# Kernel tuning notes

Hardware: AMD Instinct MI355X
Metric: run time of the kernel (lower is better)

Reference implementation:

```python
import math
import jax, jax.numpy as jnp
import numpy as np

B, T, S, D, H, L, DFF, IN, PERIOD = 16, 600, 600, 1024, 8, 8, 4096, 52, 25
HD = D // H
NEG = -1e9


def _param(key, name, shape, scale=0.02):
    k = jax.random.fold_in(key, hash(name) % (2**31))
    return jax.random.normal(k, shape, dtype=jnp.float32) * scale


def setup_inputs() -> dict:
    key = jax.random.key(0)
    k1, k2, k3 = jax.random.split(key, 3)
    inp = {}
    inp["x"] = jax.random.normal(k1, (B, T, IN), dtype=jnp.float32)
    inp["memory"] = jax.random.normal(k2, (B, S, D), dtype=jnp.float32)
    inp["timesteps"] = jax.random.randint(k3, (B,), 0, 1000, dtype=jnp.int32)

    # Periodic positional encoding buffer: sinusoidal over one period, tiled.
    pos = jnp.arange(PERIOD, dtype=jnp.float32)[:, None]
    div = jnp.exp(jnp.arange(0, D, 2, dtype=jnp.float32) * (-math.log(10000.0) / D))
    pe_p = jnp.zeros((PERIOD, D), dtype=jnp.float32)
    pe_p = pe_p.at[:, 0::2].set(jnp.sin(pos * div)).at[:, 1::2].set(jnp.cos(pos * div))
    inp["pe"] = jnp.tile(pe_p, (T // PERIOD + 1, 1))[:T]  # [T, D]

    # ALiBi-style periodic bias (vectorized form of init_bi_biased_mask_faceformer).
    # alibi[h,i,j] = -slope_h * floor((i-j)/period) for j<=i, -slope_h*floor((j-i-1)/period) for j>i
    slopes = jnp.array([0.5 ** (h + 1) for h in range(H)], dtype=jnp.float32)
    di = jnp.arange(T)[:, None] - jnp.arange(T)[None, :]
    steps = jnp.where(di >= 0, di // PERIOD, (-di - 1) // PERIOD).astype(jnp.float32)
    inp["alibi"] = -slopes[:, None, None] * steps[None]  # [H, T, T]

    # Parameters
    inp["W_in"] = _param(key, "W_in", (D, IN))
    inp["b_in"] = jnp.zeros((D,), jnp.float32)
    inp["te_W1"] = _param(key, "te_W1", (D, D))
    inp["te_b1"] = jnp.zeros((D,), jnp.float32)
    inp["te_W2"] = _param(key, "te_W2", (D, D))
    inp["te_b2"] = jnp.zeros((D,), jnp.float32)
    for nm, shape in [
        ("sa_Wqkv", (L, 3 * D, D)), ("sa_bqkv", (L, 3 * D)),
        ("sa_Wo", (L, D, D)), ("sa_bo", (L, D)),
        ("ca_Wqkv", (L, 3 * D, D)), ("ca_bqkv", (L, 3 * D)),
        ("ca_Wo", (L, D, D)), ("ca_bo", (L, D)),
        ("ff_W1", (L, DFF, D)), ("ff_b1", (L, DFF)),
        ("ff_W2", (L, D, DFF)), ("ff_b2", (L, D)),
    ]:
        inp[nm] = _param(key, nm, shape)
    for nm in ["ln1_g", "ln2_g", "ln3_g"]:
        inp[nm] = jnp.ones((L, D), jnp.float32)
    for nm in ["ln1_b", "ln2_b", "ln3_b"]:
        inp[nm] = jnp.zeros((L, D), jnp.float32)
    inp["W_out"] = _param(key, "W_out", (IN, D))
    inp["b_out"] = jnp.zeros((IN,), jnp.float32)
    return inp


def _ln(x, g, b, eps=1e-5):
    mu = jnp.mean(x, axis=-1, keepdims=True)
    var = jnp.mean(jnp.square(x - mu), axis=-1, keepdims=True)
    return (x - mu) * jax.lax.rsqrt(var + eps) * g + b


def _mha(q_in, kv_in, Wqkv, bqkv, Wo, bo, bias):
    # q_in: [B,Tq,D]; kv_in: [B,Tk,D]; bias broadcastable to [B,H,Tq,Tk]
    Wq, Wk, Wv = jnp.split(Wqkv, 3, axis=0)
    bq, bk, bv = jnp.split(bqkv, 3, axis=0)
    Bn, Tq, _ = q_in.shape
    Tk = kv_in.shape[1]
    q = (q_in @ Wq.T + bq).reshape(Bn, Tq, H, HD).transpose(0, 2, 1, 3)
    k = (kv_in @ Wk.T + bk).reshape(Bn, Tk, H, HD).transpose(0, 2, 1, 3)
    v = (kv_in @ Wv.T + bv).reshape(Bn, Tk, H, HD).transpose(0, 2, 1, 3)
    scores = jnp.einsum("bhqd,bhkd->bhqk", q, k) / math.sqrt(HD) + bias
    attn = jax.nn.softmax(scores, axis=-1)
    out = jnp.einsum("bhqk,bhkd->bhqd", attn, v)
    out = out.transpose(0, 2, 1, 3).reshape(Bn, Tq, D)
    return out @ Wo.T + bo


def reference(x, memory, timesteps, pe, alibi, W_in, b_in, te_W1, te_b1, te_W2, te_b2,
              sa_Wqkv, sa_bqkv, sa_Wo, sa_bo, ca_Wqkv, ca_bqkv, ca_Wo, ca_bo,
              ff_W1, ff_b1, ff_W2, ff_b2, ln1_g, ln1_b, ln2_g, ln2_b, ln3_g, ln3_b,
              W_out, b_out):
    # --- timestep embedding (DDPM sinusoidal + 2-layer SiLU MLP) ---
    half = D // 2
    exponent = jnp.exp(-math.log(10000.0) * jnp.arange(half, dtype=jnp.float32) / (half - 1.0))
    emb = timesteps.astype(jnp.float32)[:, None] * exponent[None, :]
    t_emb = jnp.concatenate([jnp.sin(emb), jnp.cos(emb)], axis=-1)  # [B, D]
    t_emb = jax.nn.silu(t_emb @ te_W1.T + te_b1) @ te_W2.T + te_b2
    adapter = t_emb[:, None, :]  # [B, 1, D] adapter token

    # --- input projection + periodic positional encoding ---
    h = x @ W_in.T + b_in + pe[None]  # [B, T, D]

    # --- attention biases (adapter column is always attendable => zero bias) ---
    sa_bias = jnp.concatenate([jnp.zeros((H, T, 1), jnp.float32), alibi], axis=-1)[None]  # [1,H,T,1+T]
    eye = jnp.eye(T, S, dtype=jnp.float32)
    mem_bias = jnp.where(eye > 0, 0.0, NEG)  # FaceFormer diagonal-only memory mask
    mem_bias = jnp.concatenate([jnp.zeros((T, 1), jnp.float32), mem_bias], axis=-1)[None, None]  # [1,1,T,1+S]

    # --- stacked decoder layers (post-norm, adapter prepended to K/V) ---
    for l in range(L):
        x_adpt = jnp.concatenate([adapter, h], axis=1)  # [B, 1+T, D]
        h = _ln(h + _mha(h, x_adpt, sa_Wqkv[l], sa_bqkv[l], sa_Wo[l], sa_bo[l], sa_bias), ln1_g[l], ln1_b[l])
        mem_adpt = jnp.concatenate([adapter, memory], axis=1)  # [B, 1+S, D]
        h = _ln(h + _mha(h, mem_adpt, ca_Wqkv[l], ca_bqkv[l], ca_Wo[l], ca_bo[l], mem_bias), ln2_g[l], ln2_b[l])
        ff = jax.nn.relu(h @ ff_W1[l].T + ff_b1[l]) @ ff_W2[l].T + ff_b2[l]
        h = _ln(h + ff, ln3_g[l], ln3_b[l])

    return h @ W_out.T + b_out  # [B, T, IN]
```

## Files before the change

### kernel.cpp

```cpp
#include <hip/hip_runtime.h>
#include <stdint.h>

#define B_ 16
#define T_ 600
#define S_ 600
#define D_ 1024
#define H_ 8
#define HD_ 128
#define L_ 8
#define DFF_ 4096
#define IN_ 52
#define TP1 601
#define MTOK 9600
#define MPAD 9728
#define VTK 608

typedef unsigned short u16;
typedef float f32x4 __attribute__((ext_vector_type(4)));
typedef __bf16 bf16x8 __attribute__((ext_vector_type(8)));

__device__ __forceinline__ u16 f2bf(float f){
  union { float f; unsigned u; } v; v.f = f;
  v.u += 0x7FFFu + ((v.u >> 16) & 1u);
  return (u16)(v.u >> 16);
}
__device__ __forceinline__ float bf2f(u16 h){
  union { unsigned u; float f; } v; v.u = ((unsigned)h) << 16;
  return v.f;
}
__device__ __forceinline__ void gld_lds16(const void* g, void* l){
  __builtin_amdgcn_global_load_lds(
      (const __attribute__((address_space(1))) void*)(uintptr_t)g,
      (__attribute__((address_space(3))) void*)(uintptr_t)l, 16, 0, 0);
}
__device__ __forceinline__ f32x4 MM(bf16x8 a, bf16x8 b, f32x4 c){
  return __builtin_amdgcn_mfma_f32_16x16x32_bf16(a, b, c, 0, 0, 0);
}
#define BAR() asm volatile("s_barrier" ::: "memory")

template<int EPI>
__global__ __launch_bounds__(512, 2)
void k_gemm256(const u16* __restrict__ A, const u16* __restrict__ W,
               const float* __restrict__ bias, void* __restrict__ Cout,
               int N, int K){
  __shared__ u16 lds[65536];
  const int t = threadIdx.x;
  const int w = t >> 6, l = t & 63;
  const int lr = l & 15, lg = l >> 4;
  const int wr = w >> 2, wc = w & 3;

  int lin = blockIdx.y * gridDim.x + blockIdx.x;
  const int nwg = gridDim.x * gridDim.y;
  lin = (lin & 7) * (nwg >> 3) + (lin >> 3);
  const long m0 = (long)(lin / gridDim.x) * 256;
  const long n0 = (long)(lin % gridDim.x) * 256;

  const int srow = w*8 + (l >> 3);
  const int schk = (l & 7) ^ (l >> 3);
  const u16* gA = A + (m0 + srow) * (long)K + schk * 8;
  const u16* gB = W + (n0 + srow) * (long)K + schk * 8;

  const int chk0 = ((    lg) ^ (lr & 7)) * 8;
  const int chk1 = ((4 + lg) ^ (lr & 7)) * 8;
  const int arow = (wr*128 + lr) * 64;
  const int brow = (wc*64  + lr) * 64 + 16384;

  f32x4 acc[8][4] = {};
  const int NT = K >> 6;

#define STG_A(i) gld_lds16(gA + (long)(i)*64*K + nc, (void*)(lds + nb + (i)*4096 + w*512))
#define STG_B(i) gld_lds16(gB + (long)(i)*64*K + nc, (void*)(lds + nb + 16384 + (i)*4096 + w*512))
#define LOADF(mq, CH) \
    a0 = *(const bf16x8*)(lds + bufo + arow + ((mq)*4+0)*1024 + (CH)); \
    a1 = *(const bf16x8*)(lds + bufo + arow + ((mq)*4+1)*1024 + (CH)); \
    a2 = *(const bf16x8*)(lds + bufo + arow + ((mq)*4+2)*1024 + (CH)); \
    a3 = *(const bf16x8*)(lds + bufo + arow + ((mq)*4+3)*1024 + (CH)); \
    b0 = *(const bf16x8*)(lds + bufo + brow + 0*1024 + (CH)); \
    b1 = *(const bf16x8*)(lds + bufo + brow + 1*1024 + (CH)); \
    b2 = *(const bf16x8*)(lds + bufo + brow + 2*1024 + (CH));  \
    b3 = *(const bf16x8*)(lds + bufo + brow + 3*1024 + (CH));
#define MFMA16(mq) \
    __builtin_amdgcn_s_setprio(1); \
    { const bf16x8 aa[4] = {a0,a1,a2,a3}; const bf16x8 bb4[4] = {b0,b1,b2,b3}; \
      _Pragma("unroll") for (int i_ = 0; i_ < 4; i_++) \
        _Pragma("unroll") for (int j_ = 0; j_ < 4; j_++) \
          acc[(mq)*4+i_][j_] = MM(aa[i_], bb4[j_], acc[(mq)*4+i_][j_]); } \
    __builtin_amdgcn_s_setprio(0);

  { const int nb = 0; const long nc = 0;
    STG_B(0); STG_B(1); STG_B(2); STG_B(3);
    STG_A(0); STG_A(1); STG_A(2); STG_A(3);
  }
  asm volatile("s_waitcnt vmcnt(0)" ::: "memory");
  BAR();

  int bufo = 0;
  for (int tt = 0; tt < NT; ++tt){
    const int nb = bufo ^ 32768;
    const bool st = (tt + 1 < NT);
    const long nc = (long)(tt + 1) * 64;
    bf16x8 a0,a1,a2,a3,b0,b1,b2,b3;
    LOADF(0, chk0);
    if (st){ STG_B(0); STG_B(1); STG_B(2); STG_B(3); }
    BAR();
    MFMA16(0);
    BAR();
    LOADF(0, chk1);
    if (st){ STG_A(0); STG_A(1); STG_A(2); STG_A(3); }
    BAR();
    MFMA16(0);
    BAR();
    LOADF(1, chk0);
    BAR();
    MFMA16(1);
    BAR();
    LOADF(1, chk1);
    asm volatile("s_waitcnt vmcnt(0)" ::: "memory");
    BAR();
    MFMA16(1);
    BAR();
    bufo = nb;
  }
#undef STG_A
#undef STG_B
#undef LOADF
#undef MFMA16

  const int r4 = lg * 4;
#pragma unroll
  for (int nf = 0; nf < 4; nf++){
    const int colt = wc*64 + nf*16 + lr;
    const float bv = bias[n0 + colt];
#pragma unroll
    for (int mf = 0; mf < 8; mf++){
      const int rowt = wr*128 + mf*16 + r4;
#pragma unroll
      for (int r = 0; r < 4; r++){
        float v = acc[mf][nf][r] + bv;
        if (EPI == 1) v = fmaxf(v, 0.f);
        const int row = rowt + r;
        lds[row*256 + (((colt >> 3) ^ (row & 7)) << 3) + (colt & 7)] = f2bf(v);
      }
    }
  }
  BAR();
  u16* cbase = (u16*)Cout + n0;
#pragma unroll
  for (int pass = 0; pass < 2; pass++){
#pragma unroll
    for (int it = 0; it < 8; it++){
      const int row = it*32 + w*4 + (l >> 4);
      const int ck  = (l & 15) + pass*16;
      const uint4 v = *(const uint4*)(lds + row*256 + ((ck ^ (row & 7)) << 3));
      *(uint4*)(cbase + (m0 + row) * (long)N + ck*8) = v;
    }
  }
}

template<int EPI>
__global__ __launch_bounds__(256, 4)
void k_gemm_n128(const u16* __restrict__ A, const u16* __restrict__ W,
                 const float* __restrict__ bias, void* __restrict__ Cout,
                 int N, int K){
  __shared__ u16 lds[16384];
  const int t = threadIdx.x;
  const int w = t >> 6, l = t & 63;
  const int lr = l & 15, lg = l >> 4;
  const int wr = w >> 1, wc = w & 1;

  int lin = blockIdx.y * gridDim.x + blockIdx.x;
  const int nwg = gridDim.x * gridDim.y;
  lin = (lin & 7) * (nwg >> 3) + (lin >> 3);
  const long m0 = (long)(lin / gridDim.x) * 128;
  const long n0 = (long)(lin % gridDim.x) * 128;

  const int schk = (t & 3) ^ ((t >> 3) & 3);
  const u16* gA = A + (m0 + (t >> 2)) * (long)K + schk * 8;
  const u16* gB = W + (n0 + (t >> 2)) * (long)K + schk * 8;

  const int ch = (lg ^ ((lr >> 1) & 3)) * 8;
  const int aoff = wr*2048 + lr*32 + ch;
  const int boff = 4096 + wc*2048 + lr*32 + ch;

  f32x4 acc[4][4] = {};
  const int NT = K >> 5;

#define STG128(nb, nc) \
    gld_lds16(gA + (nc),              (void*)(lds + (nb) + 0    + w*512)); \
    gld_lds16(gA + 64*(long)K + (nc), (void*)(lds + (nb) + 2048 + w*512)); \
    gld_lds16(gB + (nc),              (void*)(lds + (nb) + 4096 + w*512)); \
    gld_lds16(gB + 64*(long)K + (nc), (void*)(lds + (nb) + 6144 + w*512));

  STG128(0, 0);
  asm volatile("s_waitcnt vmcnt(0)" ::: "memory");
  BAR();

  int bufo = 0;
  for (int tt = 0; tt < NT; ++tt){
    const int nb = bufo ^ 8192;
    const bool st = (tt + 1 < NT);
    const long nc = (long)(tt + 1) * 32;
    if (st){ STG128(nb, nc); }
    bf16x8 a0,a1,a2,a3,b0,b1,b2,b3;
    a0 = *(const bf16x8*)(lds + bufo + aoff + 0*512);
    a1 = *(const bf16x8*)(lds + bufo + aoff + 1*512);
    a2 = *(const bf16x8*)(lds + bufo + aoff + 2*512);
    a3 = *(const bf16x8*)(lds + bufo + aoff + 3*512);
    b0 = *(const bf16x8*)(lds + bufo + boff + 0*512);
    b1 = *(const bf16x8*)(lds + bufo + boff + 1*512);
    b2 = *(const bf16x8*)(lds + bufo + boff + 2*512);
    b3 = *(const bf16x8*)(lds + bufo + boff + 3*512);
    __builtin_amdgcn_s_setprio(1);
    acc[0][0] = MM(a0,b0,acc[0][0]); acc[0][1] = MM(a0,b1,acc[0][1]);
    acc[0][2] = MM(a0,b2,acc[0][2]); acc[0][3] = MM(a0,b3,acc[0][3]);
    acc[1][0] = MM(a1,b0,acc[1][0]); acc[1][1] = MM(a1,b1,acc[1][1]);
    acc[1][2] = MM(a1,b2,acc[1][2]); acc[1][3] = MM(a1,b3,acc[1][3]);
    acc[2][0] = MM(a2,b0,acc[2][0]); acc[2][1] = MM(a2,b1,acc[2][1]);
    acc[2][2] = MM(a2,b2,acc[2][2]); acc[2][3] = MM(a2,b3,acc[2][3]);
    acc[3][0] = MM(a3,b0,acc[3][0]); acc[3][1] = MM(a3,b1,acc[3][1]);
    acc[3][2] = MM(a3,b2,acc[3][2]); acc[3][3] = MM(a3,b3,acc[3][3]);
    __builtin_amdgcn_s_setprio(0);
    if (st) asm volatile("s_waitcnt vmcnt(0)" ::: "memory");
    BAR();
    bufo = nb;
  }
#undef STG128

  const int r4 = lg * 4;
#pragma unroll
  for (int nf = 0; nf < 4; nf++){
    const int colt = wc*64 + nf*16 + lr;
    const float bv = bias[n0 + colt];
#pragma unroll
    for (int mf = 0; mf < 4; mf++){
      const int rowt = wr*64 + mf*16 + r4;
#pragma unroll
      for (int r = 0; r < 4; r++){
        float v = acc[mf][nf][r] + bv;
        if (EPI == 1) v = fmaxf(v, 0.f);
        const int row = rowt + r;
        lds[row*128 + (((colt >> 3) ^ (row & 7)) << 3) + (colt & 7)] = f2bf(v);
      }
    }
  }
  BAR();
  u16* cbase = (u16*)Cout + n0;
#pragma unroll
  for (int it = 0; it < 8; it++){
    const int row = it*16 + w*4 + (l >> 4);
    const int ck  = l & 15;
    const uint4 v = *(const uint4*)(lds + row*128 + ((ck ^ (row & 7)) << 3));
    *(uint4*)(cbase + (m0 + row) * (long)N + ck*8) = v;
  }
}

__global__ __launch_bounds__(256)
void k_gemm_in(const u16* __restrict__ A, const u16* __restrict__ W,
               const float* __restrict__ bias, const float* __restrict__ pe,
               float* __restrict__ hf, u16* __restrict__ hbf, u16* __restrict__ xad){
  __shared__ u16 sA[128*64];
  __shared__ u16 sB[128*64];
  const int t = threadIdx.x;
  const int w = t >> 6, l = t & 63;
  const int lr = l & 15, lg = l >> 4;
  const long m0 = (long)blockIdx.y * 128;
  const long n0 = (long)blockIdx.x * 128;
  const int wm = (w >> 1) << 6, wn = (w & 1) << 6;
  const int srow = t >> 3;
  const int schk = (t & 7) ^ (srow & 7);
  const u16* gA = A + (m0 + srow) * 64 + schk * 8;
  const u16* gB = W + (n0 + srow) * 64 + schk * 8;
#pragma unroll
  for (int i = 0; i < 4; i++){
    gld_lds16(gA + i*32*64, (void*)(sA + i*2048 + (t>>6)*512));
    gld_lds16(gB + i*32*64, (void*)(sB + i*2048 + (t>>6)*512));
  }
  asm volatile("s_waitcnt vmcnt(0)" ::: "memory");
  __syncthreads();
  f32x4 acc[4][4] = {};
#pragma unroll
  for (int kk = 0; kk < 2; kk++){
    bf16x8 af[4], bfv[4];
#pragma unroll
    for (int i = 0; i < 4; i++){
      const int row = wm + i*16 + lr;
      af[i] = *(const bf16x8*)(sA + row*64 + ((kk*4+lg)^(row&7))*8);
    }
#pragma unroll
    for (int j = 0; j < 4; j++){
      const int row = wn + j*16 + lr;
      bfv[j] = *(const bf16x8*)(sB + row*64 + ((kk*4+lg)^(row&7))*8);
    }
#pragma unroll
    for (int i = 0; i < 4; i++)
#pragma unroll
      for (int j = 0; j < 4; j++)
        acc[i][j] = MM(af[i], bfv[j], acc[i][j]);
  }
  const int r0 = lg * 4;
#pragma unroll
  for (int j = 0; j < 4; j++){
    const long col = n0 + wn + j*16 + lr;
    const float bv = bias[col];
#pragma unroll
    for (int i = 0; i < 4; i++){
      const long row = m0 + wm + i*16 + r0;
#pragma unroll
      for (int r = 0; r < 4; r++){
        const long rr = row + r;
        if (rr >= MTOK) continue;
        const float v = acc[i][j][r] + bv + pe[(rr % 25)*1024 + col];
        const u16 hv = f2bf(v);
        hf[rr*1024 + col] = v;
        hbf[rr*1024 + col] = hv;
        const long bq = rr / 600, tq = rr % 600;
        xad[((bq*TP1 + 1 + tq) << 10) + col] = hv;
      }
    }
  }
}

__global__ __launch_bounds__(256)
void k_gemm_out(const u16* __restrict__ A, const u16* __restrict__ W,
                const float* __restrict__ bias, float* __restrict__ outp){
  __shared__ u16 sA[128*32];
  __shared__ u16 sB[128*32];
  const int t = threadIdx.x;
  const int w = t >> 6, l = t & 63;
  const long m0 = (long)blockIdx.y * 128;
  const int wm = (w >> 1) << 6, wn = (w & 1) << 6;
  const int K = 1024;
  f32x4 acc[4][4] = {};
  const char* gA0 = (const char*)(A + (m0 + (t >> 2)) * (long)K) + (t & 3) * 16;
  const char* gA1 = gA0 + 64 * (long)K * 2;
  const char* gB0 = (const char*)(W + (long)(t >> 2) * K) + (t & 3) * 16;
  const char* gB1 = gB0 + 64 * (long)K * 2;
  char* lA = (char*)sA + w * 1024;
  char* lB = (char*)sB + w * 1024;
  const int lr = l & 15;
  const int lkb = (l >> 4) * 16;
  for (long k0 = 0; k0 < K; k0 += 32){
    const long kb = k0 * 2;
    gld_lds16(gA0 + kb, lA);
    gld_lds16(gA1 + kb, lA + 4096);
    gld_lds16(gB0 + kb, lB);
    gld_lds16(gB1 + kb, lB + 4096);
    __syncthreads();
    bf16x8 af[4], bfv[4];
#pragma unroll
    for (int i = 0; i < 4; i++)
      af[i] = *(const bf16x8*)((const char*)sA + (wm + i*16 + lr)*64 + lkb);
#pragma unroll
    for (int j = 0; j < 4; j++)
      bfv[j] = *(const bf16x8*)((const char*)sB + (wn + j*16 + lr)*64 + lkb);
#pragma unroll
    for (int i = 0; i < 4; i++)
#pragma unroll
      for (int j = 0; j < 4; j++)
        acc[i][j] = MM(af[i], bfv[j], acc[i][j]);
    __syncthreads();
  }
  const int r0 = (l >> 4) * 4;
#pragma unroll
  for (int j = 0; j < 4; j++){
    const int col = wn + j*16 + lr;
    if (col >= IN_) continue;
    const float bv = bias[col];
#pragma unroll
    for (int i = 0; i < 4; i++){
      const long row = m0 + wm + i*16 + r0;
#pragma unroll
      for (int r = 0; r < 4; r++)
        outp[(row + r) * (long)IN_ + col] = acc[i][j][r] + bv;
    }
  }
}

__global__ __launch_bounds__(256)
void k_vtrans(const u16* __restrict__ qkv, u16* __restrict__ vt){
  const int b = blockIdx.z;
  const int h = blockIdx.y >> 1;
  const int d0 = (blockIdx.y & 1) * 64;
  const int k0 = blockIdx.x * 64;
  __shared__ u16 tile[64][72];
  const int t = threadIdx.x;
#pragma unroll
  for (int it = 0; it < 2; it++){
    const int idx = t + it*256;
    const int kk = idx >> 3;
    const int dd = (idx & 7) * 8;
    const int kabs = k0 + kk;
    union { bf16x8 v; u16 us[8]; } u;
    if (kabs <= 600)
      u.v = *(const bf16x8*)(qkv + ((long)b*TP1 + kabs)*3072 + 2048 + h*128 + d0 + dd);
    else {
#pragma unroll
      for (int j = 0; j < 8; j++) u.us[j] = 0;
    }
    *(bf16x8*)(&tile[kk][dd]) = u.v;
  }
  __syncthreads();
#pragma unroll
  for (int it = 0; it < 2; it++){
    const int idx = t + it*256;
    const int dd = idx >> 3;
    const int kc = (idx & 7) * 8;
    if (k0 + kc + 7 < VTK){
      union { uint4 o; u16 us[8]; } u;
#pragma unroll
      for (int j = 0; j < 8; j++) u.us[j] = tile[kc + j][dd];
      *(uint4*)(vt + ((long)(b*8 + h)*128 + d0 + dd)*VTK + k0 + kc) = u.o;
    }
  }
}

__global__ __launch_bounds__(256)
void k_sa_attn3(const u16* __restrict__ qkv, const u16* __restrict__ vt,
                u16* __restrict__ outp){
  const int id = blockIdx.x;
  const int g  = id & 127;
  const int qt = id >> 7;
  const int b = g >> 3, h = g & 7;
  const int w = threadIdx.x >> 6, l = threadIdx.x & 63;
  const int lr = l & 15, lg = l >> 4;
  const int q0 = qt * 64 + w * 16;
  const float scale = 0.08838834764831845f;
  const float slope = exp2f(-(float)(h + 1));

  __shared__ u16 Kl[2][4096];
  __shared__ u16 Vl[2][4096];
  __shared__ u16 Pl[4][16*40];
  __shared__ float cS[4][16];

  const long bb = (long)b * TP1;
  const u16* qptr = qkv + (bb + 1 + q0 + lr) * 3072 + h * 128 + lg * 8;
  bf16x8 aq[4];
#pragma unroll
  for (int kk = 0; kk < 4; kk++) aq[kk] = *(const bf16x8*)(qptr + kk * 32);

  bf16x8 ones;
#pragma unroll
  for (int i = 0; i < 8; i++) ones[i] = (__bf16)1.0f;

  const int kj0 = w*2, kj1 = w*2 + 1;
  const int kkey0 = kj0*4 + (l >> 4), kkey1 = kj1*4 + (l >> 4);
  const u16* kg0 = qkv + (bb + kkey0)*3072 + 1024 + h*128 + (((l&15) ^ (kkey0&7)))*8;
  const u16* kg1 = qkv + (bb + kkey1)*3072 + 1024 + h*128 + (((l&15) ^ (kkey1&7)))*8;
  const u16* vbase = vt + (long)(b*8 + h) * 128 * VTK;
  const int vd0 = kj0*16 + (l >> 2), vd1 = kj1*16 + (l >> 2);
  const u16* vg0 = vbase + (long)vd0*VTK + ((l&3) ^ ((vd0 >> 1) & 3))*8;
  const u16* vg1 = vbase + (long)vd1*VTK + ((l&3) ^ ((vd1 >> 1) & 3))*8;

#define STAGE(buf, kb) \
  gld_lds16(kg0 + (long)(kb)*3072, (void*)(Kl[buf] + kj0*512)); \
  gld_lds16(kg1 + (long)(kb)*3072, (void*)(Kl[buf] + kj1*512)); \
  gld_lds16(vg0 + (kb),            (void*)(Vl[buf] + kj0*512)); \
  gld_lds16(vg1 + (kb),            (void*)(Vl[buf] + kj1*512));

  f32x4 o[8] = {};
  float mrow[4] = {-1e30f, -1e30f, -1e30f, -1e30f};
  float lsumq = 0.f;

  STAGE(0, 0);
  asm volatile("s_waitcnt vmcnt(0)" ::: "memory");
  BAR();

  for (int kt = 0; kt < 19; kt++){
    const int kb0 = kt * 32;
    const int cur = kt & 1;
    const bool st = (kt < 18);
    if (st){ STAGE(cur ^ 1, kb0 + 32); }
    f32x4 s0 = {}, s1 = {};
    __builtin_amdgcn_s_setprio(1);
#pragma unroll
    for (int kk = 0; kk < 4; kk++){
      const int sw = ((kk*4 + lg) ^ (lr & 7)) * 8;
      bf16x8 bk0 = *(const bf16x8*)(Kl[cur] + lr*128 + sw);
      bf16x8 bk1 = *(const bf16x8*)(Kl[cur] + (lr+16)*128 + sw);
      s0 = MM(aq[kk], bk0, s0);
      s1 = MM(aq[kk], bk1, s1);
    }
    __builtin_amdgcn_s_setprio(0);
    float v0a[4], v1a[4];
#pragma unroll
    for (int r = 0; r < 4; r++){
      const int iq = q0 + lg * 4 + r;
      float v0 = s0[r] * scale, v1 = s1[r] * scale;
      const int k0a = kb0 + lr, k1a = kb0 + 16 + lr;
      if (k0a >= 601) v0 = -1e30f;
      else if (k0a > 0){
        const int j = k0a - 1, di = iq - j;
        const int st2 = di >= 0 ? di/25 : (-di-1)/25;
        v0 -= slope * (float)st2;
      }
      if (k1a >= 601) v1 = -1e30f;
      else {
        const int j = k1a - 1, di = iq - j;
        const int st2 = di >= 0 ? di/25 : (-di-1)/25;
        v1 -= slope * (float)st2;
      }
      v0a[r] = v0; v1a[r] = v1;
    }
    bool okl = true;
#pragma unroll
    for (int r = 0; r < 4; r++)
      okl = okl && (v0a[r] <= mrow[r] + 8.f) && (v1a[r] <= mrow[r] + 8.f);
    float c = 1.f;
    bool resc = false;
    if (__all(okl)){
#pragma unroll
      for (int r = 0; r < 4; r++){
        Pl[w][(lg*4 + r)*40 + lr]      = f2bf(__expf(v0a[r] - mrow[r]));
        Pl[w][(lg*4 + r)*40 + 16 + lr] = f2bf(__expf(v1a[r] - mrow[r]));
      }
    } else {
#pragma unroll
      for (int r = 0; r < 4; r++){
        float mx = fmaxf(v0a[r], v1a[r]);
#pragma unroll
        for (int d = 8; d >= 1; d >>= 1) mx = fmaxf(mx, __shfl_xor(mx, d, 64));
        const float mnew = fmaxf(mrow[r], mx);
        const float corr = __expf(mrow[r] - mnew);
        mrow[r] = mnew;
        if (lr == 0) cS[w][lg*4 + r] = corr;
        Pl[w][(lg*4 + r)*40 + lr]      = f2bf(__expf(v0a[r] - mnew));
        Pl[w][(lg*4 + r)*40 + 16 + lr] = f2bf(__expf(v1a[r] - mnew));
      }
      c = cS[w][lr];
      resc = true;
    }
    const bf16x8 pa = *(const bf16x8*)(&Pl[w][lr*40 + lg*8]);
    f32x4 zz = {0.f, 0.f, 0.f, 0.f};
    f32x4 sacc = MM(ones, pa, zz);
    lsumq = lsumq * c + sacc[0];
    __builtin_amdgcn_s_setprio(1);
#pragma unroll
    for (int dc = 0; dc < 8; dc++){
      const int d = dc*16 + lr;
      const bf16x8 va = *(const bf16x8*)(Vl[cur] + d*32 + ((lg ^ ((d >> 1) & 3))*8));
      if (resc){
#pragma unroll
        for (int rr = 0; rr < 4; rr++) o[dc][rr] *= c;
      }
      o[dc] = MM(va, pa, o[dc]);
    }
    __builtin_amdgcn_s_setprio(0);
    if (st){
      asm volatile("s_waitcnt vmcnt(0)" ::: "memory");
      BAR();
    }
  }
#undef STAGE
  const int tq = q0 + lr;
  if (tq < 600){
    const float inv = 1.f / lsumq;
    u16* op = outp + ((long)b*600 + tq) * 1024 + h * 128;
#pragma unroll
    for (int dc = 0; dc < 8; dc++){
      union { uint2 o8; u16 us[4]; } pk;
#pragma unroll
      for (int rr = 0; rr < 4; rr++) pk.us[rr] = f2bf(o[dc][rr] * inv);
      *(uint2*)(op + dc*16 + lg*4) = pk.o8;
    }
  }
}

__global__ __launch_bounds__(256)
void k_ca_attn(const u16* __restrict__ qca, const u16* __restrict__ kv,
               u16* __restrict__ outp){
  const int wid = blockIdx.x * 4 + (threadIdx.x >> 6);
  const int l = threadIdx.x & 63;
  if (wid >= MTOK) return;
  const int b = wid / 600, t = wid % 600;
  const u16* q  = qca + (long)wid * 1024;
  const u16* ka = kv + ((long)b * TP1) * 2048;
  const u16* km = kv + ((long)(b * TP1 + 1 + t)) * 2048;
  const float scale = 0.08838834764831845f;
#pragma unroll
  for (int h = 0; h < 8; h++){
    const int d = h*128 + l*2;
    const float q0 = bf2f(q[d]),  q1 = bf2f(q[d+1]);
    float s0 = q0*bf2f(ka[d]) + q1*bf2f(ka[d+1]);
    float s1 = q0*bf2f(km[d]) + q1*bf2f(km[d+1]);
#pragma unroll
    for (int dd = 32; dd >= 1; dd >>= 1){
      s0 += __shfl_xor(s0, dd, 64);
      s1 += __shfl_xor(s1, dd, 64);
    }
    s0 *= scale; s1 *= scale;
    const float mx = fmaxf(s0, s1);
    const float e0 = __expf(s0 - mx), e1 = __expf(s1 - mx);
    const float inv = 1.f / (e0 + e1);
    const float o0 = (e0*bf2f(ka[1024+d])   + e1*bf2f(km[1024+d]))   * inv;
    const float o1 = (e0*bf2f(ka[1024+d+1]) + e1*bf2f(km[1024+d+1])) * inv;
    const unsigned pack = (unsigned)f2bf(o0) | ((unsigned)f2bf(o1) << 16);
    *(unsigned*)(outp + (long)wid*1024 + d) = pack;
  }
}

__global__ __launch_bounds__(256)
void k_ln2(float* __restrict__ hf, const u16* __restrict__ sub,
           const float* __restrict__ g, const float* __restrict__ bb,
           u16* __restrict__ hbf, u16* __restrict__ xad){
  const long m = blockIdx.x;
  const int t = threadIdx.x;
  float4* r = (float4*)(hf + m*1024);
  float4 v = r[t];
  union { uint2 u; u16 us[4]; } sv;
  sv.u = *(const uint2*)(sub + m*1024 + t*4);
  v.x += bf2f(sv.us[0]); v.y += bf2f(sv.us[1]);
  v.z += bf2f(sv.us[2]); v.w += bf2f(sv.us[3]);
  float sum = v.x + v.y + v.z + v.w;
  float sumsq = v.x*v.x + v.y*v.y + v.z*v.z + v.w*v.w;
#pragma unroll
  for (int d = 32; d >= 1; d >>= 1){ sum += __shfl_xor(sum,d,64); sumsq += __shfl_xor(sumsq,d,64); }
  __shared__ float red[8];
  const int w = t >> 6;
  if ((t & 63) == 0){ red[w] = sum; red[4+w] = sumsq; }
  __syncthreads();
  sum   = red[0]+red[1]+red[2]+red[3];
  sumsq = red[4]+red[5]+red[6]+red[7];
  const float mu  = sum * (1.f/1024.f);
  const float var = sumsq * (1.f/1024.f) - mu*mu;
  const float rstd = rsqrtf(var + 1e-5f);
  const float4 gv = ((const float4*)g)[t];
  const float4 bv = ((const float4*)bb)[t];
  float4 y;
  y.x = (v.x - mu) * rstd * gv.x + bv.x;
  y.y = (v.y - mu) * rstd * gv.y + bv.y;
  y.z = (v.z - mu) * rstd * gv.z + bv.z;
  y.w = (v.w - mu) * rstd * gv.w + bv.w;
  r[t] = y;
  union { uint2 u; u16 us[4]; } p;
  p.us[0] = f2bf(y.x); p.us[1] = f2bf(y.y); p.us[2] = f2bf(y.z); p.us[3] = f2bf(y.w);
  *(uint2*)(hbf + m*1024 + t*4) = p.u;
  if (xad){
    const long bq = m / 600, tq = m % 600;
    *(uint2*)(xad + ((bq*TP1 + 1 + tq) << 10) + t*4) = p.u;
  }
}

__global__ void k_temb_sin(const int* __restrict__ ts, float* __restrict__ emb){
  const int b = blockIdx.x;
  const float t = (float)ts[b];
  for (int j = threadIdx.x; j < 1024; j += 256){
    const int jj = j < 512 ? j : j - 512;
    const float ex = expf(-9.210340371976184f * (float)jj / 511.0f);
    const float v = t * ex;
    emb[b*1024 + j] = (j < 512) ? sinf(v) : cosf(v);
  }
}

__global__ void k_te_mm(const float* __restrict__ in, const float* __restrict__ W,
                        const float* __restrict__ bv, float* __restrict__ outp,
                        int act, u16* __restrict__ xad, u16* __restrict__ mad){
  __shared__ float row[1024];
  const int b = blockIdx.y;
  for (int k = threadIdx.x; k < 1024; k += 256) row[k] = in[b*1024 + k];
  __syncthreads();
  const int n = blockIdx.x*256 + threadIdx.x;
  const float* wr = W + (long)n*1024;
  float s = 0.f;
  for (int k = 0; k < 1024; k += 4){
    const float4 w4 = *(const float4*)(wr + k);
    s += row[k]*w4.x + row[k+1]*w4.y + row[k+2]*w4.z + row[k+3]*w4.w;
  }
  s += bv[n];
  if (act) s = s / (1.f + expf(-s));
  outp[b*1024 + n] = s;
  if (xad){
    const u16 h = f2bf(s);
    xad[((long)b*TP1)*1024 + n] = h;
    mad[((long)b*TP1)*1024 + n] = h;
  }
}

__global__ void k_convert_weights(const float* __restrict__ sqkv, const float* __restrict__ swo,
                                  const float* __restrict__ cqkv, const float* __restrict__ cwo,
                                  const float* __restrict__ fw1,  const float* __restrict__ fw2,
                                  u16* __restrict__ wbuf){
  const long idx = ((long)blockIdx.x*256 + threadIdx.x) * 8;
  const float* src; long off;
  if      (idx <  3145728L){ src = sqkv; off = idx; }
  else if (idx <  4194304L){ src = swo;  off = idx -  3145728L; }
  else if (idx <  7340032L){ src = cqkv; off = idx -  4194304L; }
  else if (idx <  8388608L){ src = cwo;  off = idx -  7340032L; }
  else if (idx < 12582912L){ src = fw1;  off = idx -  8388608L; }
  else                     { src = fw2;  off = idx - 12582912L; }
  const float4 a = *(const float4*)(src + off);
  const float4 c = *(const float4*)(src + off + 4);
  uint4 o;
  o.x = (unsigned)f2bf(a.x) | ((unsigned)f2bf(a.y) << 16);
  o.y = (unsigned)f2bf(a.z) | ((unsigned)f2bf(a.w) << 16);
  o.z = (unsigned)f2bf(c.x) | ((unsigned)f2bf(c.y) << 16);
  o.w = (unsigned)f2bf(c.z) | ((unsigned)f2bf(c.w) << 16);
  *(uint4*)(wbuf + idx) = o;
}

__global__ void k_convert_wout(const float* __restrict__ src, u16* __restrict__ dst){
  const int i = blockIdx.x*256 + threadIdx.x;
  const int row = i >> 10;
  dst[i] = (row < IN_) ? f2bf(src[i]) : (u16)0;
}

__global__ void k_convert_x(const float* __restrict__ x, u16* __restrict__ dst){
  const int i = blockIdx.x*256 + threadIdx.x;
  const int row = i >> 6, c = i & 63;
  float v = 0.f;
  if (row < MTOK && c < IN_) v = x[(long)row*IN_ + c];
  dst[i] = f2bf(v);
}

__global__ void k_convert_win(const float* __restrict__ wi, u16* __restrict__ dst){
  const int i = blockIdx.x*256 + threadIdx.x;
  const int row = i >> 6, c = i & 63;
  dst[i] = (c < IN_) ? f2bf(wi[(long)row*IN_ + c]) : (u16)0;
}

__global__ void k_build_memadpt(const float* __restrict__ mem, u16* __restrict__ mad){
  const long i = ((long)blockIdx.x*256 + threadIdx.x) * 8;
  const long tok = i >> 10, col = i & 1023;
  const long b = tok / 600, s = tok % 600;
  const float4 a = *(const float4*)(mem + i);
  const float4 c = *(const float4*)(mem + i + 4);
  uint4 o;
  o.x = (unsigned)f2bf(a.x) | ((unsigned)f2bf(a.y) << 16);
  o.y = (unsigned)f2bf(a.z) | ((unsigned)f2bf(a.w) << 16);
  o.z = (unsigned)f2bf(c.x) | ((unsigned)f2bf(c.y) << 16);
  o.w = (unsigned)f2bf(c.z) | ((unsigned)f2bf(c.w) << 16);
  *(uint4*)(mad + ((b*TP1 + 1 + s) << 10) + col) = o;
}

extern "C" void kernel_launch(void* const* d_in, const int* in_sizes, int n_in,
                              void* d_out, int out_size, void* d_ws, size_t ws_size,
                              hipStream_t stream){
  const float* x        = (const float*)d_in[0];
  const float* memory   = (const float*)d_in[1];
  const int*   tsteps   = (const int*)  d_in[2];
  const float* pe       = (const float*)d_in[3];
  const float* W_in     = (const float*)d_in[5];
  const float* b_in     = (const float*)d_in[6];
  const float* te_W1    = (const float*)d_in[7];
  const float* te_b1    = (const float*)d_in[8];
  const float* te_W2    = (const float*)d_in[9];
  const float* te_b2    = (const float*)d_in[10];
  const float* sa_Wqkv  = (const float*)d_in[11];
  const float* sa_bqkv  = (const float*)d_in[12];
  const float* sa_Wo    = (const float*)d_in[13];
  const float* sa_bo    = (const float*)d_in[14];
  const float* ca_Wqkv  = (const float*)d_in[15];
  const float* ca_bqkv  = (const float*)d_in[16];
  const float* ca_Wo    = (const float*)d_in[17];
  const float* ca_bo    = (const float*)d_in[18];
  const float* ff_W1    = (const float*)d_in[19];
  const float* ff_b1    = (const float*)d_in[20];
  const float* ff_W2    = (const float*)d_in[21];
  const float* ff_b2    = (const float*)d_in[22];
  const float* ln1_g    = (const float*)d_in[23];
  const float* ln2_g    = (const float*)d_in[24];
  const float* ln3_g    = (const float*)d_in[25];
  const float* ln1_b    = (const float*)d_in[26];
  const float* ln2_b    = (const float*)d_in[27];
  const float* ln3_b    = (const float*)d_in[28];
  const float* W_out    = (const float*)d_in[29];
  const float* b_out    = (const float*)d_in[30];

  char* ws = (char*)d_ws;
  float* h_f    = (float*)(ws + 0);
  u16*   h_bf   = (u16*)  (ws + 39321600);
  u16*   attn_bf= (u16*)  (ws + 58982400);
  u16*   xadpt  = (u16*)  (ws + 78643200);
  u16*   madpt  = (u16*)  (ws + 98336768);
  u16*   qkv    = (u16*)  (ws + 118030336);
  u16*   ffb    = (u16*)  (ws + 177799168);
  u16*   wbuf   = (u16*)  (ws + 257490944);
  u16*   sub_bf = (u16*)  (ws + 291045376);
  float* temb_a = (float*)(ws + 177799168);
  float* temb_b = (float*)(ws + 177864704);
  u16*   vtg    = (u16*)  (ws + 177799168 + 262144);
  u16*   x_bf   = wbuf;
  u16*   win_bf = wbuf + 622592;
  u16*   wout_bf= wbuf;

  u16* qca  = qkv;
  u16* kvca = qkv + (long)MPAD * 1024;

  k_temb_sin<<<dim3(16), dim3(256), 0, stream>>>(tsteps, temb_a);
  k_te_mm<<<dim3(4,16), dim3(256), 0, stream>>>(temb_a, te_W1, te_b1, temb_b, 1, (u16*)nullptr, (u16*)nullptr);
  k_te_mm<<<dim3(4,16), dim3(256), 0, stream>>>(temb_b, te_W2, te_b2, temb_a, 0, xadpt, madpt);
  k_build_memadpt<<<dim3(4800), dim3(256), 0, stream>>>(memory, madpt);
  k_convert_x<<<dim3(2432), dim3(256), 0, stream>>>(x, x_bf);
  k_convert_win<<<dim3(256), dim3(256), 0, stream>>>(W_in, win_bf);
  k_gemm_in<<<dim3(8,76), dim3(256), 0, stream>>>(x_bf, win_bf, b_in, pe, h_f, h_bf, xadpt);

  for (int l = 0; l < L_; l++){
    k_convert_weights<<<dim3(8192), dim3(256), 0, stream>>>(
        sa_Wqkv + (long)l*3145728, sa_Wo + (long)l*1048576,
        ca_Wqkv + (long)l*3145728, ca_Wo + (long)l*1048576,
        ff_W1 + (long)l*4194304,  ff_W2 + (long)l*4194304, wbuf);
    k_gemm256<0><<<dim3(12,38), dim3(512), 0, stream>>>(xadpt, wbuf, sa_bqkv + l*3072, (void*)qkv, 3072, 1024);
    k_vtrans<<<dim3(10,16,16), dim3(256), 0, stream>>>(qkv, vtg);
    k_sa_attn3<<<dim3(1280), dim3(256), 0, stream>>>(qkv, vtg, attn_bf);
    k_gemm_n128<0><<<dim3(8,76), dim3(256), 0, stream>>>(attn_bf, wbuf + 3145728, sa_bo + l*1024, (void*)sub_bf, 1024, 1024);
    k_ln2<<<dim3(9600), dim3(256), 0, stream>>>(h_f, sub_bf, ln1_g + l*1024, ln1_b + l*1024, h_bf, (u16*)nullptr);
    k_gemm_n128<0><<<dim3(8,76), dim3(256), 0, stream>>>(h_bf, wbuf + 4194304, ca_bqkv + l*3072, (void*)qca, 1024, 1024);
    k_gemm_n128<0><<<dim3(16,76), dim3(256), 0, stream>>>(madpt, wbuf + 4194304 + 1048576, ca_bqkv + l*3072 + 1024, (void*)kvca, 2048, 1024);
    k_ca_attn<<<dim3(2400), dim3(256), 0, stream>>>(qca, kvca, attn_bf);
    k_gemm_n128<0><<<dim3(8,76), dim3(256), 0, stream>>>(attn_bf, wbuf + 7340032, ca_bo + l*1024, (void*)sub_bf, 1024, 1024);
    k_ln2<<<dim3(9600), dim3(256), 0, stream>>>(h_f, sub_bf, ln2_g + l*1024, ln2_b + l*1024, h_bf, (u16*)nullptr);
    k_gemm256<1><<<dim3(16,38), dim3(512), 0, stream>>>(h_bf, wbuf + 8388608, ff_b1 + l*4096, (void*)ffb, 4096, 1024);
    k_gemm_n128<0><<<dim3(8,76), dim3(256), 0, stream>>>(ffb, wbuf + 12582912, ff_b2 + l*1024, (void*)sub_bf, 1024, 4096);
    k_ln2<<<dim3(9600), dim3(256), 0, stream>>>(h_f, sub_bf, ln3_g + l*1024, ln3_b + l*1024, h_bf, xadpt);
  }
  k_convert_wout<<<dim3(512), dim3(256), 0, stream>>>(W_out, wout_bf);
  k_gemm_out<<<dim3(1,75), dim3(256), 0, stream>>>(h_bf, wout_bf, b_out, (float*)d_out);
}
```

Before: 4.811 ms.

## Restructure GEMM main loop into half-tile staged pipeline with finer vmcnt waits

Rewrites the 256x256 GEMM main loop so that global-to-LDS loads are issued in half-K (32-column) slices, staged six slices ahead, with partial s_waitcnt vmcnt(8) instead of a full drain each K-step. The LDS layout changes to a 32-element-wide row with a new XOR swizzle, and each phase loads fragments and issues the next stage before its MFMAs. The goal is to keep more memory traffic in flight and stop stalling on a full vmcnt(0) every iteration. The trade-off is more barriers per iteration and a new swizzle that may cause LDS bank conflicts.

```diff
diff --git a/kernel.cpp b/kernel.cpp
--- a/kernel.cpp
+++ b/kernel.cpp
@@ -55,76 +55,77 @@
   const long m0 = (long)(lin / gridDim.x) * 256;
   const long n0 = (long)(lin % gridDim.x) * 256;
 
-  const int srow = w*8 + (l >> 3);
-  const int schk = (l & 7) ^ (l >> 3);
+  const int srow = t >> 2;
+  const int schk = (t & 3) ^ ((t >> 3) & 3);
   const u16* gA = A + (m0 + srow) * (long)K + schk * 8;
   const u16* gB = W + (n0 + srow) * (long)K + schk * 8;
 
-  const int chk0 = ((    lg) ^ (lr & 7)) * 8;
-  const int chk1 = ((4 + lg) ^ (lr & 7)) * 8;
-  const int arow = (wr*128 + lr) * 64;
-  const int brow = (wc*64  + lr) * 64 + 16384;
+  const int swz = (lr >> 1) & 3;
+  const int ch  = (lg ^ swz) * 8;
 
   f32x4 acc[8][4] = {};
   const int NT = K >> 6;
-
-#define STG_A(i) gld_lds16(gA + (long)(i)*64*K + nc, (void*)(lds + nb + (i)*4096 + w*512))
-#define STG_B(i) gld_lds16(gB + (long)(i)*64*K + nc, (void*)(lds + nb + 16384 + (i)*4096 + w*512))
-#define LOADF(mq, CH) \
-    a0 = *(const bf16x8*)(lds + bufo + arow + ((mq)*4+0)*1024 + (CH)); \
-    a1 = *(const bf16x8*)(lds + bufo + arow + ((mq)*4+1)*1024 + (CH)); \
-    a2 = *(const bf16x8*)(lds + bufo + arow + ((mq)*4+2)*1024 + (CH)); \
-    a3 = *(const bf16x8*)(lds + bufo + arow + ((mq)*4+3)*1024 + (CH)); \
-    b0 = *(const bf16x8*)(lds + bufo + brow + 0*1024 + (CH)); \
-    b1 = *(const bf16x8*)(lds + bufo + brow + 1*1024 + (CH)); \
-    b2 = *(const bf16x8*)(lds + bufo + brow + 2*1024 + (CH));  \
-    b3 = *(const bf16x8*)(lds + bufo + brow + 3*1024 + (CH));
-#define MFMA16(mq) \
+  const int NH = NT * 4;
+
+#define STG_HALF(s_) do { \
+    const int tt_ = (s_) >> 2; \
+    const int arr_ = (s_) & 1; \
+    const int kh_ = ((s_) >> 1) & 1; \
+    const long col_ = (long)tt_*64 + kh_*32; \
+    const u16* src_ = arr_ ? (gB + col_) : (gA + col_); \
+    u16* dst_ = lds + ((tt_ & 1) << 15) + (arr_ << 14) + (kh_ << 13) + w*512; \
+    gld_lds16(src_,                 (void*)dst_); \
+    gld_lds16(src_ + 128*(long)K,   (void*)(dst_ + 4096)); \
+  } while(0)
+
+#define PHASE(T_, Q_) do { \
+    const int kk_ = (Q_) >> 1; \
+    const int mq_ = (Q_) & 1; \
+    const int bufo_ = ((T_) & 1) << 15; \
+    const int abase_ = bufo_ + (kk_ << 13) + (wr*128 + mq_*64 + lr)*32 + ch; \
+    const int bbase_ = bufo_ + 16384 + (kk_ << 13) + (wc*64 + lr)*32 + ch; \
+    bf16x8 a0,a1,a2,a3,b0,b1,b2,b3; \
+    a0 = *(const bf16x8*)(lds + abase_ + 0*512); \
+    a1 = *(const bf16x8*)(lds + abase_ + 1*512); \
+    a2 = *(const bf16x8*)(lds + abase_ + 2*512); \
+    a3 = *(const bf16x8*)(lds + abase_ + 3*512); \
+    b0 = *(const bf16x8*)(lds + bbase_ + 0*512); \
+    b1 = *(const bf16x8*)(lds + bbase_ + 1*512); \
+    b2 = *(const bf16x8*)(lds + bbase_ + 2*512); \
+    b3 = *(const bf16x8*)(lds + bbase_ + 3*512); \
+    { const int s_ = 4*(T_) + (Q_) + 6; if (s_ < NH) STG_HALF(s_); } \
+    if ((Q_) == 1){ \
+      if ((T_) == NT-1) asm volatile("s_waitcnt vmcnt(0)" ::: "memory"); \
+      else              asm volatile("s_waitcnt vmcnt(8)" ::: "memory"); \
+    } \
+    if ((Q_) == 3 && (T_) < NT-1) asm volatile("s_waitcnt vmcnt(8)" ::: "memory"); \
+    BAR(); \
     __builtin_amdgcn_s_setprio(1); \
-    { const bf16x8 aa[4] = {a0,a1,a2,a3}; const bf16x8 bb4[4] = {b0,b1,b2,b3}; \
-      _Pragma("unroll") for (int i_ = 0; i_ < 4; i_++) \
-        _Pragma("unroll") for (int j_ = 0; j_ < 4; j_++) \
-          acc[(mq)*4+i_][j_] = MM(aa[i_], bb4[j_], acc[(mq)*4+i_][j_]); } \
-    __builtin_amdgcn_s_setprio(0);
-
-  { const int nb = 0; const long nc = 0;
-    STG_B(0); STG_B(1); STG_B(2); STG_B(3);
-    STG_A(0); STG_A(1); STG_A(2); STG_A(3);
-  }
-  asm volatile("s_waitcnt vmcnt(0)" ::: "memory");
+    acc[mq_*4+0][0] = MM(a0,b0,acc[mq_*4+0][0]); acc[mq_*4+0][1] = MM(a0,b1,acc[mq_*4+0][1]); \
+    acc[mq_*4+0][2] = MM(a0,b2,acc[mq_*4+0][2]); acc[mq_*4+0][3] = MM(a0,b3,acc[mq_*4+0][3]); \
+    acc[mq_*4+1][0] = MM(a1,b0,acc[mq_*4+1][0]); acc[mq_*4+1][1] = MM(a1,b1,acc[mq_*4+1][1]); \
+    acc[mq_*4+1][2] = MM(a1,b2,acc[mq_*4+1][2]); acc[mq_*4+1][3] = MM(a1,b3,acc[mq_*4+1][3]); \
+    acc[mq_*4+2][0] = MM(a2,b0,acc[mq_*4+2][0]); acc[mq_*4+2][1] = MM(a2,b1,acc[mq_*4+2][1]); \
+    acc[mq_*4+2][2] = MM(a2,b2,acc[mq_*4+2][2]); acc[mq_*4+2][3] = MM(a2,b3,acc[mq_*4+2][3]); \
+    acc[mq_*4+3][0] = MM(a3,b0,acc[mq_*4+3][0]); acc[mq_*4+3][1] = MM(a3,b1,acc[mq_*4+3][1]); \
+    acc[mq_*4+3][2] = MM(a3,b2,acc[mq_*4+3][2]); acc[mq_*4+3][3] = MM(a3,b3,acc[mq_*4+3][3]); \
+    __builtin_amdgcn_s_setprio(0); \
+    BAR(); \
+  } while(0)
+
+#pragma unroll
+  for (int s = 0; s < 6; ++s) STG_HALF(s);
+  asm volatile("s_waitcnt vmcnt(8)" ::: "memory");
   BAR();
 
-  int bufo = 0;
-  for (int tt = 0; tt < NT; ++tt){
-    const int nb = bufo ^ 32768;
-    const bool st = (tt + 1 < NT);
-    const long nc = (long)(tt + 1) * 64;
-    bf16x8 a0,a1,a2,a3,b0,b1,b2,b3;
-    LOADF(0, chk0);
-    if (st){ STG_B(0); STG_B(1); STG_B(2); STG_B(3); }
-    BAR();
-    MFMA16(0);
-    BAR();
-    LOADF(0, chk1);
-    if (st){ STG_A(0); STG_A(1); STG_A(2); STG_A(3); }
-    BAR();
-    MFMA16(0);
-    BAR();
-    LOADF(1, chk0);
-    BAR();
-    MFMA16(1);
-    BAR();
-    LOADF(1, chk1);
-    asm volatile("s_waitcnt vmcnt(0)" ::: "memory");
-    BAR();
-    MFMA16(1);
-    BAR();
-    bufo = nb;
-  }
-#undef STG_A
-#undef STG_B
-#undef LOADF
-#undef MFMA16
+  for (int T = 0; T < NT; ++T){
+    PHASE(T, 0);
+    PHASE(T, 1);
+    PHASE(T, 2);
+    PHASE(T, 3);
+  }
+#undef STG_HALF
+#undef PHASE
 
   const int r4 = lg * 4;
 #pragma unroll
```

Result: no change. 4.834 ms (+0.5%).
